# Kernel tuning notes

Measured on AMD Instinct MI355X. Metric: run time of the kernel, lower is better.

Reference implementation:

```python
import jax, jax.numpy as jnp
import numpy as np

LRELU = 0.01  # torch nn.LeakyReLU default slope

def _lrelu(x):
    return jnp.where(x >= 0, x, LRELU * x)

def setup_inputs() -> dict:
    key = jax.random.key(0)
    ks = jax.random.split(key, 10)
    B, Cin, Cout, H, W, K, FD, LAT = 16, 256, 256, 64, 64, 3, 128, 128
    y = jax.random.normal(ks[0], (B, Cin, H, W), jnp.float32)
    finger = jax.random.randint(ks[1], (B, FD), 0, 2).astype(jnp.float32)
    ori_weight = jax.random.normal(ks[2], (Cout, Cin, K, K), jnp.float32) * 0.05
    w_mask = jax.random.normal(ks[3], (Cout, Cin, 1, 1), jnp.float32)
    f_weight = ori_weight[None]  # param initialized as 1*ori_weight, shape [1,Cout,Cin,K,K]
    style_w1 = jax.random.normal(ks[4], (LAT, FD), jnp.float32) / np.sqrt(FD)
    style_w2 = jax.random.normal(ks[5], (2 * Cin * K * K, LAT), jnp.float32) / np.sqrt(LAT)
    ori_bias = jax.random.normal(ks[6], (Cout,), jnp.float32) * 0.05
    b_mask = jax.random.normal(ks[7], (Cout,), jnp.float32)
    f_bias = ori_bias[None]  # [1,Cout]
    bias_w1 = jax.random.normal(ks[8], (Cout, FD), jnp.float32) / np.sqrt(FD)
    bias_w2 = jax.random.normal(ks[9], (Cout, Cout), jnp.float32) / np.sqrt(Cout)
    return dict(y=y, finger=finger, ori_weight=ori_weight, w_mask=w_mask,
                f_weight=f_weight, style_w1=style_w1, style_w2=style_w2,
                ori_bias=ori_bias, b_mask=b_mask, f_bias=f_bias,
                bias_w1=bias_w1, bias_w2=bias_w2)

def reference(y, finger, ori_weight, w_mask, f_weight, style_w1, style_w2,
              ori_bias, b_mask, f_bias, bias_w1, bias_w2):
    B = y.shape[0]
    Cout, Cin, K, _ = ori_weight.shape
    relu6 = lambda v: jnp.clip(v, 0.0, 6.0)
    # mask blending coefficients (w_mask broadcasts over the KxK taps, as in .repeat)
    f_w_weight = (6.0 - relu6(w_mask)) / 6.0          # [Cout,Cin,1,1]
    f_w_bias = (6.0 - relu6(b_mask)) / 6.0            # [Cout]
    mean_ori = ori_weight.mean()
    std_ori = jnp.std(ori_weight, ddof=1)             # torch .std() is unbiased
    # ApplyStyle: finger -> LAT -> 2*Cin*K*K scale/shift applied to f_weight
    h = _lrelu(finger @ style_w1.T)                   # [B,LAT]
    style = (h @ style_w2.T).reshape(B, 2, 1, Cin, K, K)
    s_weight = f_weight * (style[:, 0] + 1.0) + style[:, 1]  # [B,Cout,Cin,K,K]
    fw = f_w_weight[None]
    w1 = (1.0 - fw) * ori_weight[None] + fw * s_weight
    # per-sample whole-tensor re-standardization to ori stats
    mean = w1.mean(axis=(1, 2, 3, 4), keepdims=True)
    std = jnp.std(w1, axis=(1, 2, 3, 4), keepdims=True, ddof=1)
    w2 = (w1 - mean) / std * std_ori + mean_ori
    new_weight = (1.0 - fw) * ori_weight[None] + fw * w2      # [B,Cout,Cin,K,K]
    # per-sample bias
    s_bias = f_bias * _lrelu(_lrelu(finger @ bias_w1.T) @ bias_w2.T)  # [B,Cout]
    new_bias = (1.0 - f_w_bias) * ori_bias + f_w_bias * s_bias        # [B,Cout]
    pad = K // 2
    def conv_one(xi, wi, bi):
        o = jax.lax.conv_general_dilated(xi[None], wi, (1, 1),
                                         [(pad, pad), (pad, pad)],
                                         dimension_numbers=('NCHW', 'OIHW', 'NCHW'))
        return o[0] + bi[:, None, None]
    return jax.vmap(conv_one)(y, new_weight, new_bias)   # [B,Cout,H,W]
```

## Files before the change

### kernel.cpp

```cpp
#include <hip/hip_runtime.h>
#include <math.h>

#define LSLOPE 0.01f

__device__ __forceinline__ float lrelu(float x){ return x >= 0.f ? x : LSLOPE * x; }

typedef __attribute__((ext_vector_type(8))) short short8;
typedef __attribute__((ext_vector_type(4))) float f32x4;

__device__ __forceinline__ unsigned short f2bf(float f){
  union { float f; unsigned u; } v; v.f = f;
  unsigned r = v.u + 0x7FFFu + ((v.u >> 16) & 1u);
  return (unsigned short)(r >> 16);
}

__device__ __forceinline__ void gload_lds16(const unsigned short* g, unsigned short* l){
  __builtin_amdgcn_global_load_lds((const __attribute__((address_space(1))) unsigned int*)(g),
                                   (__attribute__((address_space(3))) unsigned int*)(l), 16, 0, 0);
}

constexpr int B    = 16;
constexpr int CIN  = 256;
constexpr int COUT = 256;
constexpr int HH   = 64;
constexpr int WW   = 64;
constexpr int FD   = 128;
constexpr int LAT  = 128;
constexpr int WPS  = CIN * 9;
constexpr int WTOT = COUT * WPS;
constexpr int HP   = 66;

constexpr int OFF_STAT  = 0;
constexpr int OFF_BMEAN = 16;
constexpr int OFF_BSTD  = 32;
constexpr int OFF_P     = 64;
constexpr int OFF_C     = OFF_P + 11 * 8 * WPS;
constexpr int OFF_STYLE = OFF_C + 11 * WPS;
constexpr int OFF_NBIAS = OFF_STYLE + B * 2 * WPS;
constexpr int OFF_NW    = OFF_NBIAS + B * COUT;
constexpr int OFF_YTR   = OFF_NW + (B * 9 * COUT * CIN) / 2;

constexpr int PADT = 264;
constexpr int NB_YT = HP * B;
constexpr int NB_CF = 72;
constexpr int NB_SB = B * 18 + B;

__global__ __launch_bounds__(256) void k_prep1(const float* __restrict__ y, unsigned short* __restrict__ ytrp,
                                               const float* __restrict__ ow, const float* __restrict__ fwgt,
                                               const float* __restrict__ wmask, float* __restrict__ P,
                                               const float* __restrict__ finger, const float* __restrict__ sw1,
                                               const float* __restrict__ sw2, float* __restrict__ style,
                                               const float* __restrict__ bw1, const float* __restrict__ bw2,
                                               const float* __restrict__ fbias, const float* __restrict__ bmask,
                                               const float* __restrict__ obias, float* __restrict__ nbias){
  __shared__ __align__(16) char shraw[64 * PADT * 2];
  const int blk = blockIdx.x;
  const int tid = threadIdx.x;

  if (blk < NB_YT){
    unsigned short* t = (unsigned short*)shraw;
    const int ghp = blk % HP, b = blk / HP;
    unsigned short* dst = ytrp + ((size_t)b * HP + ghp) * HP * CIN;
    if (ghp == 0 || ghp == HP - 1){
      for (int c = tid; c < HP * CIN / 8; c += 256) ((uint4*)dst)[c] = (uint4){0, 0, 0, 0};
      return;
    }
    const int h = ghp - 1;
    const float* src = y + (size_t)b * CIN * HH * WW + h * WW;
    #pragma unroll
    for (int k = 0; k < 16; ++k){
      int idx = tid + k * 256;
      int ic = idx >> 4, w4 = (idx & 15) * 4;
      float4 v = *(const float4*)(src + (size_t)ic * HH * WW + w4);
      t[(w4 + 0) * PADT + ic] = f2bf(v.x);
      t[(w4 + 1) * PADT + ic] = f2bf(v.y);
      t[(w4 + 2) * PADT + ic] = f2bf(v.z);
      t[(w4 + 3) * PADT + ic] = f2bf(v.w);
    }
    __syncthreads();
    for (int c = tid; c < HP * CIN / 8; c += 256){
      int gwp = c >> 5, icg = (c & 31) * 8;
      uint4 v = (uint4){0, 0, 0, 0};
      if (gwp >= 1 && gwp <= 64) v = *(const uint4*)(&t[(gwp - 1) * PADT + icg]);
      ((uint4*)dst)[c] = v;
    }
  } else if (blk < NB_YT + NB_CF){
    const int cb = blk - NB_YT;
    const int rb = cb % 9, ob = cb / 9;
    const int rem = rb * 256 + tid;
    const int ic = rem / 9;
    float a_ow = 0.f, q_ow = 0.f, ab = 0.f, qb = 0.f;
    float a1 = 0.f, a2 = 0.f, d1 = 0.f, d2 = 0.f, d3 = 0.f, d4 = 0.f, d5 = 0.f;
    for (int oc = ob * 32; oc < ob * 32 + 32; ++oc){
      float w = ow[(size_t)oc * WPS + rem];
      float f = fwgt[(size_t)oc * WPS + rem];
      float m = wmask[oc * CIN + ic];
      float fw = (6.f - fminf(fmaxf(m, 0.f), 6.f)) * (1.f / 6.f);
      float base = w + fw * (f - w);
      float c1 = fw * f, c2 = fw;
      a_ow += w; q_ow += w * w;
      ab += base; qb += base * base;
      a1 += c1; a2 += c2;
      d1 += c1 * c1; d2 += c2 * c2; d3 += base * c1; d4 += base * c2; d5 += c1 * c2;
    }
    float* p = P + (size_t)ob * WPS + rem;
    p[(size_t)0  * 8 * WPS] = a_ow; p[(size_t)1  * 8 * WPS] = q_ow;
    p[(size_t)2  * 8 * WPS] = ab;   p[(size_t)3  * 8 * WPS] = qb;
    p[(size_t)4  * 8 * WPS] = a1;   p[(size_t)5  * 8 * WPS] = a2;
    p[(size_t)6  * 8 * WPS] = d1;   p[(size_t)7  * 8 * WPS] = d2;
    p[(size_t)8  * 8 * WPS] = d3;   p[(size_t)9  * 8 * WPS] = d4;
    p[(size_t)10 * 8 * WPS] = d5;
  } else {
    float* sh = (float*)shraw;
    const int blk2 = blk - NB_YT - NB_CF;
    if (blk2 < B * 18){
      const int b = blk2 / 18, j0 = (blk2 - b * 18) * 256;
      if (tid < LAT){
        float a = 0.f;
        const float* fg = finger + b * FD;
        const float* w = sw1 + (size_t)tid * FD;
        for (int f = 0; f < FD; ++f) a += fg[f] * w[f];
        sh[tid] = lrelu(a);
      }
      __syncthreads();
      const int j = j0 + tid;
      float a = 0.f;
      const float* w2 = sw2 + (size_t)j * LAT;
      for (int l = 0; l < LAT; ++l) a += sh[l] * w2[l];
      style[(size_t)b * 2 * WPS + j] = a;
    } else {
      const int b = blk2 - B * 18, o = tid;
      float acc = 0.f;
      for (int f = 0; f < FD; ++f) acc += finger[b * FD + f] * bw1[o * FD + f];
      sh[o] = lrelu(acc);
      __syncthreads();
      float t = 0.f;
      for (int c = 0; c < COUT; ++c) t += sh[c] * bw2[o * COUT + c];
      t = lrelu(t);
      float sb = fbias[o] * t;
      float fwb = (6.f - fminf(fmaxf(bmask[o], 0.f), 6.f)) * (1.f / 6.f);
      nbias[b * COUT + o] = (1.f - fwb) * obias[o] + fwb * sb;
    }
  }
}

__global__ void k_coeff_r(const float* __restrict__ P, float* __restrict__ C){
  const int rem = blockIdx.x * 256 + threadIdx.x;
  #pragma unroll
  for (int a = 0; a < 11; ++a){
    float v = 0.f;
    #pragma unroll
    for (int ob = 0; ob < 8; ++ob) v += P[((size_t)a * 8 + ob) * WPS + rem];
    C[(size_t)a * WPS + rem] = v;
  }
}

__global__ __launch_bounds__(256) void k_wstats(const float* __restrict__ C, const float* __restrict__ style,
                                                float* stat, float* bmean, float* bstd){
  __shared__ float rs[4][4];
  const int b = blockIdx.x, tid = threadIdx.x;
  const int lane = tid & 63, wid = tid >> 6;
  const float* st = style + (size_t)b * 2 * WPS;
  float s = 0.f, q = 0.f, so = 0.f, qo = 0.f;
  for (int k = 0; k < 9; ++k){
    int rem = k * 256 + tid;
    float aow = C[0 * WPS + rem], qow = C[1 * WPS + rem];
    float ab  = C[2 * WPS + rem], qb  = C[3 * WPS + rem];
    float a1  = C[4 * WPS + rem], a2  = C[5 * WPS + rem];
    float d1  = C[6 * WPS + rem], d2  = C[7 * WPS + rem];
    float d3  = C[8 * WPS + rem], d4  = C[9 * WPS + rem], d5 = C[10 * WPS + rem];
    float s0 = st[rem], s1 = st[WPS + rem];
    so += aow; qo += qow;
    s += ab + s0 * a1 + s1 * a2;
    q += qb + s0 * s0 * d1 + s1 * s1 * d2 + 2.f * (s0 * d3 + s1 * d4 + s0 * s1 * d5);
  }
  for (int o = 32; o > 0; o >>= 1){
    s += __shfl_down(s, o); q += __shfl_down(q, o);
    so += __shfl_down(so, o); qo += __shfl_down(qo, o);
  }
  if (lane == 0){ rs[0][wid] = s; rs[1][wid] = q; rs[2][wid] = so; rs[3][wid] = qo; }
  __syncthreads();
  if (tid == 0){
    const float N = (float)WTOT;
    float S = rs[0][0] + rs[0][1] + rs[0][2] + rs[0][3];
    float Q = rs[1][0] + rs[1][1] + rs[1][2] + rs[1][3];
    bmean[b] = S / N;
    bstd[b]  = sqrtf((Q - S * S / N) / (N - 1.f));
    if (b == 0){
      float SO = rs[2][0] + rs[2][1] + rs[2][2] + rs[2][3];
      float QO = rs[3][0] + rs[3][1] + rs[3][2] + rs[3][3];
      stat[0] = SO / N;
      stat[1] = sqrtf((QO - SO * SO / N) / (N - 1.f));
    }
  }
}

__global__ __launch_bounds__(256) void k_new_weight4(const float* __restrict__ ow, const float* __restrict__ fwgt,
                                                     const float* __restrict__ wmask, const float* __restrict__ style,
                                                     const float* __restrict__ stat, const float* __restrict__ bmean,
                                                     const float* __restrict__ bstd, unsigned short* __restrict__ nw){
  __shared__ float ows[WPS];
  __shared__ float fws[WPS];
  __shared__ float sts[2 * WPS];
  const int bi = blockIdx.x, oc = blockIdx.y;
  const int tid = threadIdx.x;
  const float mean_ori = stat[0], std_ori = stat[1];
  const float4* owr4 = (const float4*)(ow + (size_t)oc * WPS);
  const float4* fwr4 = (const float4*)(fwgt + (size_t)oc * WPS);
  #pragma unroll
  for (int i = 0; i < 3; ++i){
    int idx = tid + i * 256;
    if (idx < WPS / 4){
      ((float4*)ows)[idx] = owr4[idx];
      ((float4*)fws)[idx] = fwr4[idx];
    }
  }
  const float fw = (6.f - fminf(fmaxf(wmask[oc * CIN + tid], 0.f), 6.f)) * (1.f / 6.f);
  #pragma unroll 1
  for (int bb = 0; bb < 4; ++bb){
    const int b = bi * 4 + bb;
    __syncthreads();
    const float4* st4 = (const float4*)(style + (size_t)b * 2 * WPS);
    #pragma unroll
    for (int i = 0; i < 5; ++i){
      int idx = tid + i * 256;
      if (idx < 2 * WPS / 4) ((float4*)sts)[idx] = st4[idx];
    }
    __syncthreads();
    const float bm = bmean[b], bs = bstd[b];
    #pragma unroll
    for (int t = 0; t < 9; ++t){
      int rem = tid * 9 + t;
      float owv = ows[rem];
      float sw = fws[rem] * (sts[rem] + 1.f) + sts[WPS + rem];
      float w1 = owv + fw * (sw - owv);
      float w2 = (w1 - bm) / bs * std_ori + mean_ori;
      nw[((size_t)(b * 9 + t) * COUT + oc) * CIN + tid] = f2bf(owv + fw * (w2 - owv));
    }
  }
}

__global__ __launch_bounds__(256, 2) void k_conv_mfma11(const unsigned short* __restrict__ ytrp,
                                                        const unsigned short* __restrict__ nw,
                                                        const float* __restrict__ nbias,
                                                        float* __restrict__ out){
  __shared__ __align__(16) unsigned short Wa[3 * 128 * 32];
  __shared__ __align__(16) unsigned short Yt[288 * 32];
  __shared__ float bsh[128];

  const int bid = blockIdx.x;
  const int xcd = bid & 7;
  const int b   = ((bid >> 8) << 3) | xcd;
  const int oc0 = ((bid >> 3) & 1) * 128;
  const int hwt = (bid >> 4) & 15;
  const int tid = threadIdx.x;
  const int lane = tid & 63, wid = tid >> 6;
  const int wr = wid >> 1, wc = wid & 1;
  const int hw0 = hwt * 256;
  const int h0  = hwt * 4;

  if (tid < 128) bsh[tid] = nbias[b * COUT + oc0 + tid];

  f32x4 acc[4][8];
  #pragma unroll
  for (int i = 0; i < 4; ++i)
    #pragma unroll
    for (int j = 0; j < 8; ++j) acc[i][j] = (f32x4){0.f, 0.f, 0.f, 0.f};

  const unsigned short* nwb = nw + ((size_t)(b * 9) * COUT + oc0) * CIN;
  const unsigned short* ytb = ytrp + (size_t)b * HP * HP * CIN;

  int a_tap[6], a_go[6], a_lo[6];
  #pragma unroll
  for (int s = 0; s < 6; ++s){
    int I = wid + 4 * s;
    int tap = I >> 3, rowbase = (I & 7) * 16;
    int row = rowbase + (lane >> 2), p = lane & 3;
    int g = p ^ ((row >> 1) & 3);
    a_tap[s] = tap;
    a_go[s]  = row * CIN + g * 8;
    a_lo[s]  = (tap * 128 + rowbase) * 32;
  }
  int y_go[5], y_lo[5]; bool y_has[5];
  #pragma unroll
  for (int s = 0; s < 5; ++s){
    int I = wid + 4 * s;
    y_has[s] = (I < 18);
    int Ic = y_has[s] ? I : 0;
    int site = Ic * 16 + (lane >> 2);
    int srow = site / 72;
    int scol = site - srow * 72;
    int gwp  = scol > 65 ? 65 : scol;
    int p = lane & 3, g = p ^ ((site >> 1) & 3);
    y_go[s] = ((h0 + srow + 1) * HP + gwp) * CIN + g * 8;
    y_lo[s] = Ic * 16 * 32;
  }

  const int gq = lane >> 4;
  int a_rb[4];
  #pragma unroll
  for (int mi = 0; mi < 4; ++mi){
    int r = wr * 64 + mi * 16 + (lane & 15);
    a_rb[mi] = r * 64 + ((gq ^ ((r >> 1) & 3)) << 4);
  }
  int b_site[8];
  #pragma unroll
  for (int ni = 0; ni < 8; ++ni)
    b_site[ni] = (wc * 2 + (ni >> 2)) * 72 + (ni & 3) * 16 + (lane & 15);

  #define STAGE(IT)                                                                 \
    {                                                                               \
      const int dhb = (IT) >> 3;                                                    \
      const int ic0s = ((IT) & 7) * 32;                                             \
      const unsigned short* ybase = ytb + (ptrdiff_t)(dhb - 1) * HP * CIN + ic0s;   \
      _Pragma("unroll")                                                             \
      for (int s = 0; s < 5; ++s)                                                   \
        if (y_has[s]) gload_lds16(ybase + y_go[s], &Yt[0] + y_lo[s]);               \
      const unsigned short* atap = nwb + (size_t)(dhb * 3) * COUT * CIN + ic0s;     \
      _Pragma("unroll")                                                             \
      for (int s = 0; s < 6; ++s)                                                   \
        gload_lds16(atap + (size_t)a_tap[s] * COUT * CIN + a_go[s], &Wa[0] + a_lo[s]); \
    }

  #define COMPUTE()                                                                 \
    {                                                                               \
      const char* wap = (const char*)&Wa[0];                                        \
      const char* ytp = (const char*)&Yt[0];                                        \
      _Pragma("unroll")                                                             \
      for (int tap = 0; tap < 3; ++tap){                                            \
        short8 af[4];                                                               \
        _Pragma("unroll")                                                           \
        for (int mi = 0; mi < 4; ++mi)                                              \
          af[mi] = *(const short8*)(wap + tap * 8192 + a_rb[mi]);                   \
        _Pragma("unroll")                                                           \
        for (int ni = 0; ni < 8; ++ni){                                             \
          const int site = b_site[ni] + tap;                                        \
          const int boff = (site << 6) + ((gq ^ ((site >> 1) & 3)) << 4);           \
          const short8 bf = *(const short8*)(ytp + boff);                           \
          _Pragma("unroll")                                                         \
          for (int mi = 0; mi < 4; ++mi)                                            \
            acc[mi][ni] = __builtin_amdgcn_mfma_f32_16x16x32_bf16(af[mi], bf, acc[mi][ni], 0, 0, 0); \
        }                                                                           \
      }                                                                             \
    }

  #pragma unroll 1
  for (int it = 0; it < 24; ++it){
    __syncthreads();
    STAGE(it);
    __syncthreads();
    COMPUTE();
  }
  #undef STAGE
  #undef COMPUTE

  const int col_l = lane & 15, row_l = (lane >> 4) * 4;
  #pragma unroll
  for (int mi = 0; mi < 4; ++mi){
    #pragma unroll
    for (int r = 0; r < 4; ++r){
      const int ocl = wr * 64 + mi * 16 + row_l + r;
      const float bb = bsh[ocl];
      float* op = out + ((size_t)(b * COUT + oc0 + ocl)) * (HH * WW) + hw0 + wc * 128;
      #pragma unroll
      for (int ni = 0; ni < 8; ++ni)
        op[(ni >> 2) * 64 + (ni & 3) * 16 + col_l] = acc[mi][ni][r] + bb;
    }
  }
}

extern "C" void kernel_launch(void* const* d_in, const int* in_sizes, int n_in,
                              void* d_out, int out_size, void* d_ws, size_t ws_size,
                              hipStream_t stream){
  const float* y      = (const float*)d_in[0];
  const float* finger = (const float*)d_in[1];
  const float* ow     = (const float*)d_in[2];
  const float* wmask  = (const float*)d_in[3];
  const float* fwgt   = (const float*)d_in[4];
  const float* sw1    = (const float*)d_in[5];
  const float* sw2    = (const float*)d_in[6];
  const float* obias  = (const float*)d_in[7];
  const float* bmask  = (const float*)d_in[8];
  const float* fbias  = (const float*)d_in[9];
  const float* bw1    = (const float*)d_in[10];
  const float* bw2    = (const float*)d_in[11];
  float* out = (float*)d_out;
  float* ws  = (float*)d_ws;

  float* stat  = ws + OFF_STAT;
  float* bmean = ws + OFF_BMEAN;
  float* bstd  = ws + OFF_BSTD;
  float* P     = ws + OFF_P;
  float* C     = ws + OFF_C;
  float* style = ws + OFF_STYLE;
  float* nbias = ws + OFF_NBIAS;
  unsigned short* nw   = (unsigned short*)(ws + OFF_NW);
  unsigned short* ytrp = (unsigned short*)(ws + OFF_YTR);

  k_prep1<<<NB_YT + NB_CF + NB_SB, 256, 0, stream>>>(y, ytrp, ow, fwgt, wmask, P,
                                                     finger, sw1, sw2, style,
                                                     bw1, bw2, fbias, bmask, obias, nbias);
  k_coeff_r<<<9, 256, 0, stream>>>(P, C);
  k_wstats<<<B, 256, 0, stream>>>(C, style, stat, bmean, bstd);
  k_new_weight4<<<dim3(B / 4, COUT), 256, 0, stream>>>(ow, fwgt, wmask, style, stat, bmean, bstd, nw);
  k_conv_mfma11<<<512, 256, 0, stream>>>(ytrp, nw, nbias, out);
}
```

Baseline: 129.2 us.

## Stage six padded input rows once per channel block, reuse across three kernel rows

The conv loop previously restaged a 4-row input tile for each of the 3 kernel-row offsets per 32-channel block. Now it loads a 6-row halo tile once per channel block and indexes it with a row offset for each of the three weight-row stages. This cuts global-to-LDS input traffic by roughly half. In exchange, LDS usage grows and each channel block carries more barriers, since the weight stages are still serialized.

```diff
diff --git a/kernel.cpp b/kernel.cpp
--- a/kernel.cpp
+++ b/kernel.cpp
@@ -240,12 +240,12 @@
   }
 }
 
-__global__ __launch_bounds__(256, 2) void k_conv_mfma11(const unsigned short* __restrict__ ytrp,
+__global__ __launch_bounds__(256, 2) void k_conv_mfma15(const unsigned short* __restrict__ ytrp,
                                                         const unsigned short* __restrict__ nw,
                                                         const float* __restrict__ nbias,
                                                         float* __restrict__ out){
   __shared__ __align__(16) unsigned short Wa[3 * 128 * 32];
-  __shared__ __align__(16) unsigned short Yt[288 * 32];
+  __shared__ __align__(16) unsigned short Yt[6 * 72 * 32];
   __shared__ float bsh[128];
 
   const int bid = blockIdx.x;
@@ -281,18 +281,18 @@
     a_go[s]  = row * CIN + g * 8;
     a_lo[s]  = (tap * 128 + rowbase) * 32;
   }
-  int y_go[5], y_lo[5]; bool y_has[5];
-  #pragma unroll
-  for (int s = 0; s < 5; ++s){
+  int y_go[7], y_lo[7]; bool y_has[7];
+  #pragma unroll
+  for (int s = 0; s < 7; ++s){
     int I = wid + 4 * s;
-    y_has[s] = (I < 18);
+    y_has[s] = (I < 27);
     int Ic = y_has[s] ? I : 0;
     int site = Ic * 16 + (lane >> 2);
     int srow = site / 72;
     int scol = site - srow * 72;
     int gwp  = scol > 65 ? 65 : scol;
     int p = lane & 3, g = p ^ ((site >> 1) & 3);
-    y_go[s] = ((h0 + srow + 1) * HP + gwp) * CIN + g * 8;
+    y_go[s] = ((h0 + srow) * HP + gwp) * CIN + g * 8;
     y_lo[s] = Ic * 16 * 32;
   }
 
@@ -308,21 +308,23 @@
   for (int ni = 0; ni < 8; ++ni)
     b_site[ni] = (wc * 2 + (ni >> 2)) * 72 + (ni & 3) * 16 + (lane & 15);
 
-  #define STAGE(IT)                                                                 \
+  #define STAGE_Y(IC0)                                                              \
     {                                                                               \
-      const int dhb = (IT) >> 3;                                                    \
-      const int ic0s = ((IT) & 7) * 32;                                             \
-      const unsigned short* ybase = ytb + (ptrdiff_t)(dhb - 1) * HP * CIN + ic0s;   \
+      const unsigned short* ybase = ytb + (IC0);                                    \
       _Pragma("unroll")                                                             \
-      for (int s = 0; s < 5; ++s)                                                   \
+      for (int s = 0; s < 7; ++s)                                                   \
         if (y_has[s]) gload_lds16(ybase + y_go[s], &Yt[0] + y_lo[s]);               \
-      const unsigned short* atap = nwb + (size_t)(dhb * 3) * COUT * CIN + ic0s;     \
+    }
+
+  #define STAGE_A(D, IC0)                                                           \
+    {                                                                               \
+      const unsigned short* atap = nwb + (size_t)((D) * 3) * COUT * CIN + (IC0);    \
       _Pragma("unroll")                                                             \
       for (int s = 0; s < 6; ++s)                                                   \
         gload_lds16(atap + (size_t)a_tap[s] * COUT * CIN + a_go[s], &Wa[0] + a_lo[s]); \
     }
 
-  #define COMPUTE()                                                                 \
+  #define COMPUTE(D)                                                                \
     {                                                                               \
       const char* wap = (const char*)&Wa[0];                                        \
       const char* ytp = (const char*)&Yt[0];                                        \
@@ -334,7 +336,7 @@
           af[mi] = *(const short8*)(wap + tap * 8192 + a_rb[mi]);                   \
         _Pragma("unroll")                                                           \
         for (int ni = 0; ni < 8; ++ni){                                             \
-          const int site = b_site[ni] + tap;                                        \
+          const int site = b_site[ni] + (D) * 72 + tap;                             \
           const int boff = (site << 6) + ((gq ^ ((site >> 1) & 3)) << 4);           \
           const short8 bf = *(const short8*)(ytp + boff);                           \
           _Pragma("unroll")                                                         \
@@ -345,13 +347,24 @@
     }
 
   #pragma unroll 1
-  for (int it = 0; it < 24; ++it){
-    __syncthreads();
-    STAGE(it);
-    __syncthreads();
-    COMPUTE();
-  }
-  #undef STAGE
+  for (int icb = 0; icb < 8; ++icb){
+    const int ic0 = icb * 32;
+    __syncthreads();
+    STAGE_Y(ic0);
+    STAGE_A(0, ic0);
+    __syncthreads();
+    COMPUTE(0);
+    __syncthreads();
+    STAGE_A(1, ic0);
+    __syncthreads();
+    COMPUTE(1);
+    __syncthreads();
+    STAGE_A(2, ic0);
+    __syncthreads();
+    COMPUTE(2);
+  }
+  #undef STAGE_Y
+  #undef STAGE_A
   #undef COMPUTE
 
   const int col_l = lane & 15, row_l = (lane >> 4) * 4;
@@ -403,5 +416,5 @@
   k_coeff_r<<<9, 256, 0, stream>>>(P, C);
   k_wstats<<<B, 256, 0, stream>>>(C, style, stat, bmean, bstd);
   k_new_weight4<<<dim3(B / 4, COUT), 256, 0, stream>>>(ow, fwgt, wmask, style, stat, bmean, bstd, nw);
-  k_conv_mfma11<<<512, 256, 0, stream>>>(ytrp, nw, nbias, out);
-}
+  k_conv_mfma15<<<512, 256, 0, stream>>>(ytrp, nw, nbias, out);
+}
```

Result: no change. 131.0 us (+1.4%).
